# Performance work log

Hardware: AMD Instinct MI355X
Metric: run time of the kernel (lower is better)

Reference implementation:

```python
import jax, jax.numpy as jnp
import numpy as np

# Config matching init_kwargs
PCR = (-51.2, -51.2, -5.0, 51.2, 51.2, 3.0)  # point cloud range
PS = 0.2                                      # pillar size
GW = int(round((PCR[3] - PCR[0]) / PS))       # 512 bev width
GH = int(round((PCR[4] - PCR[1]) / PS))       # 512 bev height
B = 4
N = 800000
CIN = 4
COUT = 32


def setup_inputs() -> dict:
    key = jax.random.key(0)
    k1, k2, k3 = jax.random.split(key, 3)
    u = jax.random.uniform(k1, (N, 3), dtype=jnp.float32)
    # points uniformly inside the point cloud range
    lo = jnp.array([PCR[0], PCR[1], PCR[2]], dtype=jnp.float32)
    ext = jnp.array([PCR[3] - PCR[0], PCR[4] - PCR[1], PCR[5] - PCR[2]], dtype=jnp.float32)
    xyz = u * ext + lo
    xyz_batch_cnt = jnp.full((B,), N // B, dtype=jnp.int32)
    pt_feature = jax.random.normal(k2, (N, CIN), dtype=jnp.float32)
    W = jax.random.normal(k3, (CIN + 3, COUT), dtype=jnp.float32) * 0.1  # xavier-ish shared MLP
    return {"xyz": xyz, "xyz_batch_cnt": xyz_batch_cnt, "pt_feature": pt_feature, "W": W}


def reference(xyz, xyz_batch_cnt, pt_feature, W):
    # point -> batch index (FGPillarQueryAndGroup grouping)
    b_idx = jnp.repeat(jnp.arange(B, dtype=jnp.int32), xyz_batch_cnt, total_repeat_length=N)
    # point -> pillar (x,y) cell
    px = jnp.clip(jnp.floor((xyz[:, 0] - PCR[0]) / PS).astype(jnp.int32), 0, GW - 1)
    py = jnp.clip(jnp.floor((xyz[:, 1] - PCR[1]) / PS).astype(jnp.int32), 0, GH - 1)
    # pillar centers; relative offsets are the grouped geometric features
    cx = (px.astype(xyz.dtype) + 0.5) * PS + PCR[0]
    cy = (py.astype(xyz.dtype) + 0.5) * PS + PCR[1]
    cz = 0.5 * (PCR[2] + PCR[5])
    offs = jnp.stack([xyz[:, 0] - cx, xyz[:, 1] - cy, xyz[:, 2] - cz], axis=1)  # (N,3)
    group_features = jnp.concatenate([pt_feature, offs], axis=1)               # (N, CIN+3)
    # shared MLP (1x1 conv == linear) + ReLU
    h = jax.nn.relu(group_features @ W)                                        # (N, COUT)
    # scatter-max pooling over pillar segments (dense BEV layout: b*H*W + y*W + x)
    seg = b_idx * (GH * GW) + py * GW + px
    pooled = jax.ops.segment_max(h, seg, num_segments=B * GH * GW)             # (B*H*W, COUT)
    pooled = jnp.where(jnp.isfinite(pooled), pooled, jnp.zeros((), pooled.dtype))
    return pooled
```

## Files before the change

### kernel.cpp

```cpp
#include <hip/hip_runtime.h>


#define GW 512
#define GH 512
#define COUT 32
#define PTS_PER_BLOCK 8

__global__ __launch_bounds__(256) void pillar_fwd(
    const float* __restrict__ xyz,
    const int*   __restrict__ cnt,
    const float4* __restrict__ feat,
    const float* __restrict__ W,
    unsigned int* __restrict__ out,
    int N, int B)
{
    __shared__ float sW[7 * COUT];
    int tid = threadIdx.x;
    if (tid < 7 * COUT) sW[tid] = W[tid];
    __syncthreads();

    int p = blockIdx.x * PTS_PER_BLOCK + (tid >> 5);
    int c = tid & 31;
    if (p >= N) return;

    float x = xyz[3 * p + 0];
    float y = xyz[3 * p + 1];
    float z = xyz[3 * p + 2];

    int b = 0, acc = 0;
    for (int k = 0; k < B; ++k) {
        acc += cnt[k];
        b += (p >= acc) ? 1 : 0;
    }

    int px = (int)floorf((x - (-51.2f)) / 0.2f);
    int py = (int)floorf((y - (-51.2f)) / 0.2f);
    px = min(max(px, 0), GW - 1);
    py = min(max(py, 0), GH - 1);

    float cx = ((float)px + 0.5f) * 0.2f + (-51.2f);
    float cy = ((float)py + 0.5f) * 0.2f + (-51.2f);
    float g4 = x - cx;
    float g5 = y - cy;
    float g6 = z + 1.0f;

    float4 f = feat[p];

    float h = f.x * sW[0 * COUT + c]
            + f.y * sW[1 * COUT + c]
            + f.z * sW[2 * COUT + c]
            + f.w * sW[3 * COUT + c]
            + g4  * sW[4 * COUT + c]
            + g5  * sW[5 * COUT + c]
            + g6  * sW[6 * COUT + c];
    h = fmaxf(h, 0.0f);

    unsigned int seg = (unsigned int)b * (GH * GW) + (unsigned int)py * GW + (unsigned int)px;
    atomicMax(out + (size_t)seg * COUT + c, __float_as_uint(h));
}

extern "C" void kernel_launch(void* const* d_in, const int* in_sizes, int n_in,
                              void* d_out, int out_size, void* d_ws, size_t ws_size,
                              hipStream_t stream) {
    const float*  xyz  = (const float*)d_in[0];
    const int*    cnt  = (const int*)d_in[1];
    const float4* feat = (const float4*)d_in[2];
    const float*  W    = (const float*)d_in[3];
    unsigned int* out  = (unsigned int*)d_out;

    int N = in_sizes[0] / 3;
    int B = in_sizes[1];

    hipMemsetAsync(d_out, 0, (size_t)out_size * sizeof(float), stream);

    int grid = (N + PTS_PER_BLOCK - 1) / PTS_PER_BLOCK;
    pillar_fwd<<<grid, 256, 0, stream>>>(xyz, cnt, feat, W, out, N, B);
}
```

Before: 252.7 us.

## Replace per-channel atomicMax scatter with counting-sort bucketing and per-pillar pooling

The single kernel did one atomicMax per point per channel into the dense output. It is replaced by four passes: count points per pillar, prefix-scan the counts into offsets, scatter compact per-point records into pillar order, then a gather pass that runs the MLP and max per pillar and writes every output cell once. This cuts global atomics to one or two per point and drops the separate output memset. In exchange it adds a 4-way launch chain, a workspace of about 8 MB of counts and cursors plus 32 bytes per point, and extra record traffic. The old path is kept as a fallback when the workspace is too small.

```diff
diff --git a/kernel.cpp b/kernel.cpp
--- a/kernel.cpp
+++ b/kernel.cpp
@@ -4,15 +4,143 @@
 #define GW 512
 #define GH 512
 #define COUT 32
+
+__device__ __forceinline__ int batch_of(int p, const int* __restrict__ cnt, int B) {
+    int b = 0, acc = 0;
+    for (int k = 0; k < B; ++k) { acc += cnt[k]; b += (p >= acc) ? 1 : 0; }
+    return b;
+}
+
+__device__ __forceinline__ void cell_of(float x, float y, int& px, int& py) {
+    px = (int)floorf((x - (-51.2f)) / 0.2f);
+    py = (int)floorf((y - (-51.2f)) / 0.2f);
+    px = min(max(px, 0), GW - 1);
+    py = min(max(py, 0), GH - 1);
+}
+
+__global__ __launch_bounds__(256) void pass_count(
+    const float* __restrict__ xyz, const int* __restrict__ cnt,
+    unsigned* __restrict__ counts, int N, int B)
+{
+    int p = blockIdx.x * 256 + threadIdx.x;
+    if (p >= N) return;
+    float x = xyz[3 * p + 0];
+    float y = xyz[3 * p + 1];
+    int px, py; cell_of(x, y, px, py);
+    int b = batch_of(p, cnt, B);
+    unsigned seg = (unsigned)b * (GH * GW) + (unsigned)py * GW + (unsigned)px;
+    atomicAdd(&counts[seg], 1u);
+}
+
+__global__ __launch_bounds__(256) void pass_scan(
+    const unsigned* __restrict__ counts, unsigned* __restrict__ cursor,
+    unsigned* __restrict__ gcur, int ncells)
+{
+    __shared__ unsigned waveOff[4];
+    __shared__ unsigned blockBase;
+    int tid = threadIdx.x;
+    int base = (blockIdx.x * 256 + tid) * 4;
+
+    uint4 cv = make_uint4(0u, 0u, 0u, 0u);
+    if (base + 3 < ncells) {
+        cv = *(const uint4*)(counts + base);
+    } else if (base < ncells) {
+        cv.x = counts[base];
+        if (base + 1 < ncells) cv.y = counts[base + 1];
+        if (base + 2 < ncells) cv.z = counts[base + 2];
+    }
+    unsigned lsum = cv.x + cv.y + cv.z + cv.w;
+
+    unsigned s = lsum;
+    int lane = tid & 63;
+    #pragma unroll
+    for (int d = 1; d < 64; d <<= 1) {
+        unsigned t = __shfl_up(s, d, 64);
+        if (lane >= d) s += t;
+    }
+    int wv = tid >> 6;
+    if (lane == 63) waveOff[wv] = s;
+    __syncthreads();
+    if (tid == 0) {
+        unsigned w0 = waveOff[0], w1 = waveOff[1], w2 = waveOff[2], w3 = waveOff[3];
+        blockBase = atomicAdd(gcur, w0 + w1 + w2 + w3);
+        waveOff[0] = 0; waveOff[1] = w0; waveOff[2] = w0 + w1; waveOff[3] = w0 + w1 + w2;
+    }
+    __syncthreads();
+
+    unsigned start = blockBase + waveOff[wv] + (s - lsum);
+    uint4 o;
+    o.x = start;
+    o.y = o.x + cv.x;
+    o.z = o.y + cv.y;
+    o.w = o.z + cv.z;
+    if (base + 3 < ncells) {
+        *(uint4*)(cursor + base) = o;
+    } else if (base < ncells) {
+        cursor[base] = o.x;
+        if (base + 1 < ncells) cursor[base + 1] = o.y;
+        if (base + 2 < ncells) cursor[base + 2] = o.z;
+    }
+}
+
+__global__ __launch_bounds__(256) void pass_scatter(
+    const float* __restrict__ xyz, const int* __restrict__ cnt,
+    const float4* __restrict__ feat,
+    unsigned* __restrict__ cursor, float4* __restrict__ records,
+    int N, int B)
+{
+    int p = blockIdx.x * 256 + threadIdx.x;
+    if (p >= N) return;
+    float x = xyz[3 * p + 0];
+    float y = xyz[3 * p + 1];
+    float z = xyz[3 * p + 2];
+    int px, py; cell_of(x, y, px, py);
+    int b = batch_of(p, cnt, B);
+    float cx = ((float)px + 0.5f) * 0.2f + (-51.2f);
+    float cy = ((float)py + 0.5f) * 0.2f + (-51.2f);
+    float4 f = feat[p];
+    unsigned seg = (unsigned)b * (GH * GW) + (unsigned)py * GW + (unsigned)px;
+    unsigned slot = atomicAdd(&cursor[seg], 1u);
+    records[(size_t)2 * slot + 0] = f;
+    records[(size_t)2 * slot + 1] = make_float4(x - cx, y - cy, z + 1.0f, 0.0f);
+}
+
+__global__ __launch_bounds__(256) void pass_pool(
+    const unsigned* __restrict__ counts, const unsigned* __restrict__ cursor,
+    const float* __restrict__ W, const float4* __restrict__ records,
+    float* __restrict__ out, int ncells)
+{
+    int tid = threadIdx.x;
+    int cell = blockIdx.x * 8 + (tid >> 5);
+    int c = tid & 31;
+    if (cell >= ncells) return;
+
+    float w0 = W[0 * COUT + c], w1 = W[1 * COUT + c], w2 = W[2 * COUT + c];
+    float w3 = W[3 * COUT + c], w4 = W[4 * COUT + c], w5 = W[5 * COUT + c];
+    float w6 = W[6 * COUT + c];
+
+    unsigned end = cursor[cell];
+    unsigned num = counts[cell];
+    unsigned i = end - num;
+
+    float best = 0.0f;
+    for (; i < end; ++i) {
+        float4 f = records[(size_t)2 * i + 0];
+        float4 g = records[(size_t)2 * i + 1];
+        float h = f.x * w0 + f.y * w1 + f.z * w2 + f.w * w3
+                + g.x * w4 + g.y * w5 + g.z * w6;
+        best = fmaxf(best, h);
+    }
+    out[(size_t)cell * COUT + c] = best;
+}
+
+
 #define PTS_PER_BLOCK 8
 
 __global__ __launch_bounds__(256) void pillar_fwd(
-    const float* __restrict__ xyz,
-    const int*   __restrict__ cnt,
-    const float4* __restrict__ feat,
-    const float* __restrict__ W,
-    unsigned int* __restrict__ out,
-    int N, int B)
+    const float* __restrict__ xyz, const int* __restrict__ cnt,
+    const float4* __restrict__ feat, const float* __restrict__ W,
+    unsigned int* __restrict__ out, int N, int B)
 {
     __shared__ float sW[7 * COUT];
     int tid = threadIdx.x;
@@ -26,36 +154,17 @@
     float x = xyz[3 * p + 0];
     float y = xyz[3 * p + 1];
     float z = xyz[3 * p + 2];
-
-    int b = 0, acc = 0;
-    for (int k = 0; k < B; ++k) {
-        acc += cnt[k];
-        b += (p >= acc) ? 1 : 0;
-    }
-
-    int px = (int)floorf((x - (-51.2f)) / 0.2f);
-    int py = (int)floorf((y - (-51.2f)) / 0.2f);
-    px = min(max(px, 0), GW - 1);
-    py = min(max(py, 0), GH - 1);
-
+    int b = batch_of(p, cnt, B);
+    int px, py; cell_of(x, y, px, py);
     float cx = ((float)px + 0.5f) * 0.2f + (-51.2f);
     float cy = ((float)py + 0.5f) * 0.2f + (-51.2f);
-    float g4 = x - cx;
-    float g5 = y - cy;
-    float g6 = z + 1.0f;
-
     float4 f = feat[p];
-
-    float h = f.x * sW[0 * COUT + c]
-            + f.y * sW[1 * COUT + c]
-            + f.z * sW[2 * COUT + c]
-            + f.w * sW[3 * COUT + c]
-            + g4  * sW[4 * COUT + c]
-            + g5  * sW[5 * COUT + c]
-            + g6  * sW[6 * COUT + c];
+    float h = f.x * sW[0 * COUT + c] + f.y * sW[1 * COUT + c]
+            + f.z * sW[2 * COUT + c] + f.w * sW[3 * COUT + c]
+            + (x - cx) * sW[4 * COUT + c] + (y - cy) * sW[5 * COUT + c]
+            + (z + 1.0f) * sW[6 * COUT + c];
     h = fmaxf(h, 0.0f);
-
-    unsigned int seg = (unsigned int)b * (GH * GW) + (unsigned int)py * GW + (unsigned int)px;
+    unsigned seg = (unsigned)b * (GH * GW) + (unsigned)py * GW + (unsigned)px;
     atomicMax(out + (size_t)seg * COUT + c, __float_as_uint(h));
 }
 
@@ -66,13 +175,35 @@
     const int*    cnt  = (const int*)d_in[1];
     const float4* feat = (const float4*)d_in[2];
     const float*  W    = (const float*)d_in[3];
-    unsigned int* out  = (unsigned int*)d_out;
 
     int N = in_sizes[0] / 3;
     int B = in_sizes[1];
-
-    hipMemsetAsync(d_out, 0, (size_t)out_size * sizeof(float), stream);
-
-    int grid = (N + PTS_PER_BLOCK - 1) / PTS_PER_BLOCK;
-    pillar_fwd<<<grid, 256, 0, stream>>>(xyz, cnt, feat, W, out, N, B);
-}
+    int ncells = B * GH * GW;
+
+    size_t offCounts  = 256;
+    size_t offCursor  = offCounts + (size_t)ncells * 4;
+    size_t offRecords = (offCursor + (size_t)ncells * 4 + 255) & ~(size_t)255;
+    size_t needed     = offRecords + (size_t)N * 32;
+
+    if (ws_size >= needed) {
+        char* ws = (char*)d_ws;
+        unsigned* gcur    = (unsigned*)ws;
+        unsigned* counts  = (unsigned*)(ws + offCounts);
+        unsigned* cursor  = (unsigned*)(ws + offCursor);
+        float4*   records = (float4*)(ws + offRecords);
+
+        hipMemsetAsync(ws, 0, offCursor, stream);
+
+        int gpts = (N + 255) / 256;
+        pass_count<<<gpts, 256, 0, stream>>>(xyz, cnt, counts, N, B);
+        pass_scan<<<(ncells + 1023) / 1024, 256, 0, stream>>>(counts, cursor, gcur, ncells);
+        pass_scatter<<<gpts, 256, 0, stream>>>(xyz, cnt, feat, cursor, records, N, B);
+        pass_pool<<<(ncells + 7) / 8, 256, 0, stream>>>(counts, cursor, W, records,
+                                                        (float*)d_out, ncells);
+    } else {
+        hipMemsetAsync(d_out, 0, (size_t)out_size * sizeof(float), stream);
+        int grid = (N + PTS_PER_BLOCK - 1) / PTS_PER_BLOCK;
+        pillar_fwd<<<grid, 256, 0, stream>>>(xyz, cnt, feat, W,
+                                             (unsigned int*)d_out, N, B);
+    }
+}
```

Result: slower. 319.7 us (+26.5%).
